# Kernel tuning notes

Measured on AMD Instinct MI355X. Metric: run time of the kernel, lower is better.

The kernel has to match this reference:

```python
import jax, jax.numpy as jnp
import numpy as np

PI = 3.1415927410125732
N = 4096
VELOCITY = 5e-7
RC = 3.15e-6          # collision radius
RR = 8e-6             # repulsion radius
RO = 2.5e-5           # orientation radius (Ra = inf -> inside_Ra all-true)
ALPHA = PI            # field of view; < 2*pi so within_view masking is active
DT_TRANS = 1.4e-14    # translational diffusion DT
DR = 0.0028
GAMMA = 25.0
DT = 0.2              # timestep dt
COLLISION_ITERS = 3   # fixed-iteration version of recursive solve_collisions
EPS = 1e-14


def _c(x):  # [N,2] real -> complex64
    return jax.lax.complex(x[..., 0], x[..., 1])


def _r(z):  # complex -> [..., 2] real
    return jnp.stack([z.real, z.imag], axis=-1)


def _anglediff(a, b):
    # torch get_anglediff: wrap angle(a)-angle(b) into (-pi, pi)
    diff = jnp.angle(a) - jnp.angle(b)
    diff = jnp.where(diff <= -PI, jnp.mod(diff, PI), diff)
    return diff - (diff >= PI) * (2.0 * PI)


def _cossim(a, b):
    # nn.CosineSimilarity(dim=1, eps=1e-14) on view_as_real of complex vectors
    dot = a.real * b.real + a.imag * b.imag
    na = jnp.sqrt(a.real ** 2 + a.imag ** 2 + 1e-30)
    nb = jnp.sqrt(b.real ** 2 + b.imag ** 2 + 1e-30)
    return dot / (jnp.maximum(na, EPS) * jnp.maximum(nb, EPS))


def setup_inputs() -> dict:
    key = jax.random.key(0)
    k1, k2, k3, k4, k5 = jax.random.split(key, 5)
    positions = jax.random.normal(k1, (N, 2), jnp.float32) * 5e-4
    ang = jax.random.uniform(k2, (N,), jnp.float32, -PI, PI)
    orientations = jnp.stack([jnp.cos(ang), jnp.sin(ang)], axis=-1)  # unit complex
    Deltas = jax.random.uniform(k3, (1,), jnp.float32, 0.1, 0.6)
    rot_noise = jax.random.normal(k4, (N,), jnp.float32)
    trans_noise = jax.random.normal(k5, (N, 2), jnp.float32)
    return {"positions": positions, "orientations": orientations, "Deltas": Deltas,
            "rot_noise": rot_noise, "trans_noise": trans_noise}


def reference(positions, orientations, Deltas, rot_noise, trans_noise):
    p = _c(positions)      # [N] complex positions
    u = _c(orientations)   # [N] complex orientations
    n = p.shape[0]
    eye = jnp.eye(n, dtype=bool)

    # pairwise direction/distance: dirs[i,j] = p_j - p_i
    dirs = p[None, :] - p[:, None]
    dists = jnp.abs(dirs)

    inside_Rr = (dists <= RR) & ~eye
    inside_Ro = dists <= RO + RC
    # inside_Ra with Ra = inf is all-True

    # angle between separation vector and orientation of the *neighbor* j
    ang_diff = _anglediff(dirs, u[None, :])
    in_front = ang_diff < PI / 2
    within_view = ang_diff < ALPHA  # alpha < 2*pi branch active

    cdtype = p.dtype
    mask_rr = (inside_Rr & in_front).astype(cdtype)
    mask_ra = within_view.astype(cdtype)  # inside_Ra all True
    mask_ro = (inside_Ro & within_view).astype(cdtype)

    n_r = mask_rr.real.sum(axis=1)
    S = (mask_rr @ p) / jnp.maximum(n_r, 1.0) - p * jnp.sign(n_r)
    d = -S

    n_a = mask_ra.real.sum(axis=1)
    cms = (mask_ra @ p) / jnp.maximum(n_a, 1.0)
    Ps = cms - p * jnp.sign(n_a)

    orientation_sums = mask_ro @ u

    leftturns = Ps * jnp.exp(1j * Deltas)
    rightturns = Ps * jnp.exp(-1j * Deltas)

    # T >= T_release branch: pick the turn most aligned with neighbor orientations
    left_closer = _cossim(leftturns, orientation_sums) >= _cossim(rightturns, orientation_sums)
    best_turns = jnp.where(left_closer, leftturns, rightturns)

    d_abs = jnp.abs(d)
    d_safe = jnp.where(d_abs > 0, d, jnp.ones((), cdtype))
    best_safe = jnp.where(jnp.abs(best_turns) > 0, best_turns, jnp.ones((), cdtype))
    angle_to_target = jnp.where(d_abs > 0, _anglediff(d_safe, u), _anglediff(best_safe, u))

    # rotational_noise = randn * sqrt(2*DR); rotation = exp(i*(dt*Gamma*DR*sin + noise*sqrt(dt)))
    rot = jnp.exp(1j * (DT * GAMMA * DR * jnp.sin(angle_to_target)
                        + rot_noise * np.float32(np.sqrt(2 * DR)) * np.float32(np.sqrt(DT))))

    # complex-normal translational noise (per-component std 1/sqrt(2)) * sqrt(2*DT) * sqrt(dt)
    tn = _c(trans_noise) * np.float32(np.sqrt(0.5)) * np.float32(np.sqrt(2 * DT_TRANS))
    translation = DT * VELOCITY * u + tn * np.float32(np.sqrt(DT))

    def collide(i, pos):
        dd = pos[None, :] - pos[:, None]
        dd_nd = jnp.where(eye, jnp.ones((), pos.dtype), dd)  # avoid 0/0 on diagonal
        ab = jnp.where(eye, 0.0, jnp.abs(dd_nd))
        coll = ab <= 2 * RC - jnp.eye(n, dtype=ab.dtype)
        safe = jnp.where(coll, ab, 1.0)
        move = jnp.where(coll, dd / safe * ((2.1 * RC - ab) * 0.5), jnp.zeros((), pos.dtype))
        return pos - move.sum(axis=1)

    new_p = jax.lax.fori_loop(0, COLLISION_ITERS, collide, p + translation)
    new_u = u * rot

    # pack the 5 complex outputs as real [5, N, 2]
    return jnp.stack([_r(new_p), _r(new_u), _r(orientation_sums), _r(leftturns), _r(rightturns)], axis=0)
```

## Files before the change

### kernel.cpp

```cpp
#include <hip/hip_runtime.h>
#include <math.h>

#define NPART 4096
#define NBLK  1024
#define NTHR  256
#define IPB   4
#define SMAX  256
#define PPT   (NPART / NTHR)

constexpr float RORC   = (float)(2.5e-5 + 3.15e-6);
constexpr float RORC2  = RORC * RORC;
constexpr float RRF    = 8e-6f;
constexpr float RR2    = RRF * RRF;
constexpr float TWORC  = (float)(2.0 * 3.15e-6);
constexpr float TWORC2 = TWORC * TWORC;
constexpr float C21RC  = (float)(2.1 * 3.15e-6);
constexpr float RCAND2 = 1.6e-9f;
constexpr float C_ROT  = (float)(0.2 * 25.0 * 0.0028);
constexpr float C_RN1  = (float)0.07483314773547883;
constexpr float C_SQDT = (float)0.4472135954999579;
constexpr float C_TRV  = (float)(0.2 * 5e-7);
constexpr float C_HALF = (float)0.7071067811865476;
constexpr float C_SQ2T = (float)1.6733200530681511e-07;
constexpr float EPSF   = 1e-14f;

__global__ __launch_bounds__(NTHR, 8) void fused_all(
        const float2* __restrict__ pos, const float2* __restrict__ ori,
        const float* __restrict__ Deltas, const float* __restrict__ rot_noise,
        const float2* __restrict__ trans_noise, float2* __restrict__ out) {
    __shared__ float    sred[2 * NTHR];
    __shared__ float    res[5][IPB];
    __shared__ unsigned bmap[NPART / 32];
    __shared__ int      Sidx[SMAX];
    __shared__ float4   posS4[SMAX / 2];
    __shared__ int      scnt;
    float2* posS = (float2*)posS4;
    const float4* __restrict__ pos4 = (const float4*)pos;

    const int tid  = threadIdx.x;
    const int il   = tid >> 6;
    const int lane = tid & 63;
    const int gi   = blockIdx.x * IPB + il;

    if (tid == 0) scnt = IPB;
    if (tid < IPB) Sidx[tid] = blockIdx.x * IPB + tid;
    if (tid < NPART / 32) bmap[tid] = 0u;

    float mx = 0.f, my = 0.f;
    #pragma unroll
    for (int k = 0; k < PPT; ++k) {
        const float2 v = pos[k * NTHR + tid];
        mx += v.x; my += v.y;
    }
    sred[tid] = mx; sred[NTHR + tid] = my;
    __syncthreads();

    const float2 pi = pos[gi];
    float nr = 0.f, sx = 0.f, sy = 0.f, oxs = 0.f, oys = 0.f;
    #pragma unroll 2
    for (int t = lane; t < NPART / 2; t += 64) {
        const float4 w = pos4[t];
        const float dx0 = w.x - pi.x, dy0 = w.y - pi.y;
        const float r20 = fmaf(dx0, dx0, dy0 * dy0);
        const float dx1 = w.z - pi.x, dy1 = w.w - pi.y;
        const float r21 = fmaf(dx1, dx1, dy1 * dy1);
        if (r20 <= RCAND2) {
            const int j = 2 * t;
            atomicOr(&bmap[j >> 5], 1u << (j & 31));
            if (r20 <= RORC2) {
                const float2 uj = ori[j];
                oxs += uj.x; oys += uj.y;
                if (r20 <= RR2 && r20 > 0.f) {
                    const float dt_ = fmaf(dx0, uj.x, dy0 * uj.y);
                    const float cr_ = fmaf(dy0, uj.x, -dx0 * uj.y);
                    if (!((dt_ <= 0.f) && (cr_ >= 0.f))) {
                        nr += 1.f; sx += w.x; sy += w.y;
                    }
                }
            }
        }
        if (r21 <= RCAND2) {
            const int j = 2 * t + 1;
            atomicOr(&bmap[j >> 5], 1u << (j & 31));
            if (r21 <= RORC2) {
                const float2 uj = ori[j];
                oxs += uj.x; oys += uj.y;
                if (r21 <= RR2 && r21 > 0.f) {
                    const float dt_ = fmaf(dx1, uj.x, dy1 * uj.y);
                    const float cr_ = fmaf(dy1, uj.x, -dx1 * uj.y);
                    if (!((dt_ <= 0.f) && (cr_ >= 0.f))) {
                        nr += 1.f; sx += w.z; sy += w.w;
                    }
                }
            }
        }
    }
    {
        float vals[5] = {nr, sx, sy, oxs, oys};
        #pragma unroll
        for (int q = 0; q < 5; ++q)
            #pragma unroll
            for (int off = 32; off >= 1; off >>= 1)
                vals[q] += __shfl_down(vals[q], off);
        if (lane == 0) {
            res[0][il] = vals[0]; res[1][il] = vals[1]; res[2][il] = vals[2];
            res[3][il] = vals[3]; res[4][il] = vals[4];
        }
    }
    __syncthreads();

    if (tid < NPART / 32) {
        unsigned bits = bmap[tid];
        if (tid == (int)(blockIdx.x >> 3))
            bits &= ~(0xFu << ((blockIdx.x & 7) * 4));
        while (bits) {
            const int b = __ffs(bits) - 1;
            bits &= bits - 1;
            const int slot = atomicAdd(&scnt, 1);
            if (slot < SMAX) Sidx[slot] = tid * 32 + b;
        }
    }
    __syncthreads();
    const int nS = (scnt < SMAX) ? scnt : SMAX;

    if (tid < nS) {
        const int p = Sidx[tid];
        const float2 pq = pos[p];
        const float2 uu = ori[p];
        const float2 tn = trans_noise[p];
        posS[tid] = make_float2(
            pq.x + (C_TRV * uu.x + ((tn.x * C_HALF) * C_SQ2T) * C_SQDT),
            pq.y + (C_TRV * uu.y + ((tn.y * C_HALF) * C_SQ2T) * C_SQDT));
    }

    for (int s = NTHR / 2; s > 0; s >>= 1) {
        if (tid < s) { sred[tid] += sred[tid + s]; sred[NTHR + tid] += sred[NTHR + tid + s]; }
        __syncthreads();
    }
    const float cmx = sred[0]    * (1.f / NPART);
    const float cmy = sred[NTHR] * (1.f / NPART);

    if (tid < IPB) {
        const int g2 = blockIdx.x * IPB + tid;
        const float2 p = pos[g2];
        const float2 u = ori[g2];
        const float nrv = res[0][tid], sxv = res[1][tid], syv = res[2][tid];
        const float osx = res[3][tid], osy = res[4][tid];

        const float inv = 1.f / fmaxf(nrv, 1.f);
        const float sg  = (nrv > 0.f) ? 1.f : 0.f;
        const float Sx = sxv * inv - p.x * sg;
        const float Sy = syv * inv - p.y * sg;
        const float dxv = -Sx, dyv = -Sy;

        const float Psx = cmx - p.x;
        const float Psy = cmy - p.y;

        float sd, cd;
        sincosf(Deltas[0], &sd, &cd);
        const float Lx = Psx * cd - Psy * sd;
        const float Ly = Psx * sd + Psy * cd;
        const float Rx = Psx * cd + Psy * sd;
        const float Ry = Psy * cd - Psx * sd;

        const float no  = fmaxf(sqrtf(osx * osx + osy * osy + 1e-30f), EPSF);
        const float nl  = fmaxf(sqrtf(Lx * Lx + Ly * Ly + 1e-30f), EPSF);
        const float nrr = fmaxf(sqrtf(Rx * Rx + Ry * Ry + 1e-30f), EPSF);
        const float csl = (Lx * osx + Ly * osy) / (nl * no);
        const float csr = (Rx * osx + Ry * osy) / (nrr * no);
        const bool left = (csl >= csr);
        const float bx = left ? Lx : Rx;
        const float by = left ? Ly : Ry;

        float cx, cy;
        if (dxv != 0.f || dyv != 0.f)    { cx = dxv; cy = dyv; }
        else if (bx != 0.f || by != 0.f) { cx = bx;  cy = by;  }
        else                             { cx = 1.f; cy = 0.f; }

        const float dt_ = cx * u.x + cy * u.y;
        const float cr_ = cy * u.x - cx * u.y;
        const float sin_t = cr_ / sqrtf(dt_ * dt_ + cr_ * cr_);

        const float ang = C_ROT * sin_t + (rot_noise[g2] * C_RN1) * C_SQDT;
        float sa, ca;
        sincosf(ang, &sa, &ca);
        out[1 * NPART + g2] = make_float2(u.x * ca - u.y * sa,
                                          u.x * sa + u.y * ca);
        out[2 * NPART + g2] = make_float2(osx, osy);
        out[3 * NPART + g2] = make_float2(Lx, Ly);
        out[4 * NPART + g2] = make_float2(Rx, Ry);
    }
    __syncthreads();

    for (int pass = 0; pass < 3; ++pass) {
        float px = 0.f, py = 0.f, ax = 0.f, ay = 0.f;
        const bool mv = (tid < nS);
        if (mv) { px = posS[tid].x; py = posS[tid].y; }
        int b = 0;
        for (; b + 4 <= nS; b += 4) {
            const float4 w0 = posS4[(b >> 1)];
            const float4 w1 = posS4[(b >> 1) + 1];
            const float bxs[4] = {w0.x, w0.z, w1.x, w1.z};
            const float bys[4] = {w0.y, w0.w, w1.y, w1.w};
            #pragma unroll
            for (int s = 0; s < 4; ++s) {
                if (mv) {
                    const float dx = bxs[s] - px, dy = bys[s] - py;
                    const float r2 = fmaf(dx, dx, dy * dy);
                    if (r2 <= TWORC2 && r2 > 0.f) {
                        const float ab = sqrtf(r2);
                        const float sc = (C21RC - ab) * 0.5f / ab;
                        ax = fmaf(dx, sc, ax);
                        ay = fmaf(dy, sc, ay);
                    }
                }
            }
        }
        for (; b < nS; ++b) {
            const float2 pb = posS[b];
            if (mv) {
                const float dx = pb.x - px, dy = pb.y - py;
                const float r2 = fmaf(dx, dx, dy * dy);
                if (r2 <= TWORC2 && r2 > 0.f) {
                    const float ab = sqrtf(r2);
                    const float sc = (C21RC - ab) * 0.5f / ab;
                    ax = fmaf(dx, sc, ax);
                    ay = fmaf(dy, sc, ay);
                }
            }
        }
        __syncthreads();
        if (mv) posS[tid] = make_float2(px - ax, py - ay);
        __syncthreads();
    }
    if (tid < IPB)
        out[0 * NPART + blockIdx.x * IPB + tid] = posS[tid];
}

extern "C" void kernel_launch(void* const* d_in, const int* in_sizes, int n_in,
                              void* d_out, int out_size, void* d_ws, size_t ws_size,
                              hipStream_t stream) {
    const float2* pos = (const float2*)d_in[0];
    const float2* ori = (const float2*)d_in[1];
    const float*  del = (const float*)d_in[2];
    const float*  rn  = (const float*)d_in[3];
    const float2* tn  = (const float2*)d_in[4];
    float2* o2 = (float2*)d_out;
    (void)d_ws; (void)ws_size;

    fused_all<<<dim3(NBLK), dim3(NTHR), 0, stream>>>(pos, ori, del, rn, tn, o2);
}
```

Baseline: 85.84 us.

## Cut barriers, merge centroid reduction into other phases, unroll neighbor scan by four

```diff
diff --git a/kernel.cpp b/kernel.cpp
--- a/kernel.cpp
+++ b/kernel.cpp
@@ -24,7 +24,7 @@
 constexpr float C_SQ2T = (float)1.6733200530681511e-07;
 constexpr float EPSF   = 1e-14f;
 
-__global__ __launch_bounds__(NTHR, 8) void fused_all(
+__global__ __launch_bounds__(NTHR, 6) void fused_all(
         const float2* __restrict__ pos, const float2* __restrict__ ori,
         const float* __restrict__ Deltas, const float* __restrict__ rot_noise,
         const float2* __restrict__ trans_noise, float2* __restrict__ out) {
@@ -42,33 +42,31 @@
     const int lane = tid & 63;
     const int gi   = blockIdx.x * IPB + il;
 
+    const float2 pi   = pos[gi];
+    const float  delv = Deltas[0];
+    float rn_early = 0.f;
+    if (tid < IPB) rn_early = rot_noise[blockIdx.x * IPB + tid];
+    {
+        const float2 ow = ori[tid * PPT];
+        const float2 tw = trans_noise[tid * PPT];
+        asm volatile("" :: "v"(ow.x), "v"(tw.x));
+    }
+
     if (tid == 0) scnt = IPB;
     if (tid < IPB) Sidx[tid] = blockIdx.x * IPB + tid;
     if (tid < NPART / 32) bmap[tid] = 0u;
-
-    float mx = 0.f, my = 0.f;
-    #pragma unroll
-    for (int k = 0; k < PPT; ++k) {
-        const float2 v = pos[k * NTHR + tid];
-        mx += v.x; my += v.y;
-    }
-    sred[tid] = mx; sred[NTHR + tid] = my;
-    __syncthreads();
-
-    const float2 pi = pos[gi];
+    __syncthreads();
+
     float nr = 0.f, sx = 0.f, sy = 0.f, oxs = 0.f, oys = 0.f;
-    #pragma unroll 2
-    for (int t = lane; t < NPART / 2; t += 64) {
-        const float4 w = pos4[t];
+    auto pair2 = [&](const float4& w, int jbase) {
         const float dx0 = w.x - pi.x, dy0 = w.y - pi.y;
         const float r20 = fmaf(dx0, dx0, dy0 * dy0);
         const float dx1 = w.z - pi.x, dy1 = w.w - pi.y;
         const float r21 = fmaf(dx1, dx1, dy1 * dy1);
         if (r20 <= RCAND2) {
-            const int j = 2 * t;
-            atomicOr(&bmap[j >> 5], 1u << (j & 31));
+            atomicOr(&bmap[jbase >> 5], 1u << (jbase & 31));
             if (r20 <= RORC2) {
-                const float2 uj = ori[j];
+                const float2 uj = ori[jbase];
                 oxs += uj.x; oys += uj.y;
                 if (r20 <= RR2 && r20 > 0.f) {
                     const float dt_ = fmaf(dx0, uj.x, dy0 * uj.y);
@@ -80,10 +78,10 @@
             }
         }
         if (r21 <= RCAND2) {
-            const int j = 2 * t + 1;
-            atomicOr(&bmap[j >> 5], 1u << (j & 31));
+            const int j1 = jbase + 1;
+            atomicOr(&bmap[j1 >> 5], 1u << (j1 & 31));
             if (r21 <= RORC2) {
-                const float2 uj = ori[j];
+                const float2 uj = ori[j1];
                 oxs += uj.x; oys += uj.y;
                 if (r21 <= RR2 && r21 > 0.f) {
                     const float dt_ = fmaf(dx1, uj.x, dy1 * uj.y);
@@ -94,6 +92,16 @@
                 }
             }
         }
+    };
+    for (int t0 = lane; t0 < NPART / 2; t0 += 256) {
+        const float4 w0 = pos4[t0];
+        const float4 w1 = pos4[t0 + 64];
+        const float4 w2 = pos4[t0 + 128];
+        const float4 w3 = pos4[t0 + 192];
+        pair2(w0, 2 * t0);
+        pair2(w1, 2 * (t0 + 64));
+        pair2(w2, 2 * (t0 + 128));
+        pair2(w3, 2 * (t0 + 192));
     }
     {
         float vals[5] = {nr, sx, sy, oxs, oys};
@@ -107,9 +115,19 @@
             res[3][il] = vals[3]; res[4][il] = vals[4];
         }
     }
-    __syncthreads();
-
-    if (tid < NPART / 32) {
+
+    float mx = 0.f, my = 0.f;
+    #pragma unroll
+    for (int k = 0; k < PPT; ++k) {
+        const float2 v = pos[k * NTHR + tid];
+        mx += v.x; my += v.y;
+    }
+    sred[tid] = mx; sred[NTHR + tid] = my;
+    __syncthreads();
+
+    if (tid < 128) {
+        sred[tid]        += sred[tid + 128];
+        sred[NTHR + tid] += sred[NTHR + tid + 128];
         unsigned bits = bmap[tid];
         if (tid == (int)(blockIdx.x >> 3))
             bits &= ~(0xFu << ((blockIdx.x & 7) * 4));
@@ -123,6 +141,10 @@
     __syncthreads();
     const int nS = (scnt < SMAX) ? scnt : SMAX;
 
+    if (tid < 64) {
+        sred[tid]        += sred[tid + 64];
+        sred[NTHR + tid] += sred[NTHR + tid + 64];
+    }
     if (tid < nS) {
         const int p = Sidx[tid];
         const float2 pq = pos[p];
@@ -132,13 +154,20 @@
             pq.x + (C_TRV * uu.x + ((tn.x * C_HALF) * C_SQ2T) * C_SQDT),
             pq.y + (C_TRV * uu.y + ((tn.y * C_HALF) * C_SQ2T) * C_SQDT));
     }
-
-    for (int s = NTHR / 2; s > 0; s >>= 1) {
-        if (tid < s) { sred[tid] += sred[tid + s]; sred[NTHR + tid] += sred[NTHR + tid + s]; }
-        __syncthreads();
-    }
-    const float cmx = sred[0]    * (1.f / NPART);
-    const float cmy = sred[NTHR] * (1.f / NPART);
+    __syncthreads();
+
+    float cmx = 0.f, cmy = 0.f;
+    if (il == 0) {
+        float vx = sred[lane];
+        float vy = sred[NTHR + lane];
+        #pragma unroll
+        for (int off = 32; off >= 1; off >>= 1) {
+            vx += __shfl_down(vx, off);
+            vy += __shfl_down(vy, off);
+        }
+        cmx = __shfl(vx, 0) * (1.f / NPART);
+        cmy = __shfl(vy, 0) * (1.f / NPART);
+    }
 
     if (tid < IPB) {
         const int g2 = blockIdx.x * IPB + tid;
@@ -157,7 +186,7 @@
         const float Psy = cmy - p.y;
 
         float sd, cd;
-        sincosf(Deltas[0], &sd, &cd);
+        sincosf(delv, &sd, &cd);
         const float Lx = Psx * cd - Psy * sd;
         const float Ly = Psx * sd + Psy * cd;
         const float Rx = Psx * cd + Psy * sd;
@@ -181,7 +210,7 @@
         const float cr_ = cy * u.x - cx * u.y;
         const float sin_t = cr_ / sqrtf(dt_ * dt_ + cr_ * cr_);
 
-        const float ang = C_ROT * sin_t + (rot_noise[g2] * C_RN1) * C_SQDT;
+        const float ang = C_ROT * sin_t + (rn_early * C_RN1) * C_SQDT;
         float sa, ca;
         sincosf(ang, &sa, &ca);
         out[1 * NPART + g2] = make_float2(u.x * ca - u.y * sa,
@@ -190,7 +219,6 @@
         out[3 * NPART + g2] = make_float2(Lx, Ly);
         out[4 * NPART + g2] = make_float2(Rx, Ry);
     }
-    __syncthreads();
 
     for (int pass = 0; pass < 3; ++pass) {
         float px = 0.f, py = 0.f, ax = 0.f, ay = 0.f;
```

New measurement: 84.55 us. No clear change (-1.5%).
